# Performance work log

Hardware: AMD Instinct MI355X
Metric: run time of the kernel (lower is better)

The kernel has to match this reference:

```python
import jax, jax.numpy as jnp
import numpy as np

B, S, H, E = 8, 4096, 1024, 8
TEMPERATURE = 1.0


def setup_inputs() -> dict:
    key = jax.random.key(0)
    ks = jax.random.split(key, 7)
    s_h = 1.0 / np.sqrt(H).astype(np.float32)
    s_h2 = 1.0 / np.sqrt(H // 2).astype(np.float32)
    return {
        "hidden_states": jax.random.normal(ks[0], (B, S, H), jnp.float32),
        # routing_network: Linear(H, H//2) -> ReLU -> Linear(H//2, E)
        "W1": jax.random.normal(ks[1], (H, H // 2), jnp.float32) * s_h,
        "b1": jnp.zeros((H // 2,), jnp.float32),
        "W2": jax.random.normal(ks[2], (H // 2, E), jnp.float32) * s_h2,
        "b2": jnp.zeros((E,), jnp.float32),
        # per-expert dense transform (fixed stand-in for torch.randn-per-call)
        "expert_W": jax.random.normal(ks[3], (E, H, H), jnp.float32) * s_h,
        "expert_b": jax.random.normal(ks[4], (E, H), jnp.float32),
    }


def reference(hidden_states, W1, b1, W2, b2, expert_W, expert_b):
    # Routing network -> logits [B, S, E]
    h = jax.nn.relu(jnp.einsum("bsh,hf->bsf", hidden_states, W1) + b1)
    logits = jnp.einsum("bsf,fe->bse", h, W2) + b2
    probs = jax.nn.softmax(logits / TEMPERATURE, axis=-1)
    # top-1 expert per token (scores are NOT applied to output in the original)
    sel = jnp.argmax(probs, axis=-1)  # [B, S] int
    out = jnp.zeros_like(hidden_states)
    for e in range(E):  # small fixed loop over experts
        mask = (sel == e)[..., None].astype(hidden_states.dtype)  # [B, S, 1]
        xe = hidden_states * mask
        ye = jnp.einsum("bsh,hd->bsd", xe, expert_W[e]) + expert_b[e]
        out = out + ye * mask
    return out
```

## Files before the change

kernel.cpp:

```cpp
#include <hip/hip_runtime.h>
#include <hip/hip_bf16.h>
#include <stdint.h>

#define NTOK 32768
#define HD 1024
#define FD 512
#define NEXP 8
#define TAU 0.05f
#define TAU2 4e-4f

typedef __attribute__((ext_vector_type(8))) short short8;
typedef __attribute__((ext_vector_type(4))) float f32x4;

__device__ __forceinline__ short f2bh(float f) {
  uint32_t u = __float_as_uint(f);
  return (short)((u + 0x7fffu + ((u >> 16) & 1u)) >> 16);
}
__device__ __forceinline__ float bh2f(short h) {
  return __uint_as_float(((uint32_t)(uint16_t)h) << 16);
}

__device__ __forceinline__ void gl16(void* lds, const void* g) {
  __builtin_amdgcn_global_load_lds(
      (const __attribute__((address_space(1))) void*)g,
      (__attribute__((address_space(3))) void*)lds, 16, 0, 0);
}

__global__ __launch_bounds__(256) void k_convert(const float* __restrict__ x,
                                                 short* __restrict__ xbf) {
  size_t i = ((size_t)blockIdx.x * 256 + threadIdx.x) * 8;
  f32x4 v0 = *(const f32x4*)(x + i);
  f32x4 v1 = *(const f32x4*)(x + i + 4);
  short8 o;
#pragma unroll
  for (int q = 0; q < 4; ++q) { o[q] = f2bh(v0[q]); o[4 + q] = f2bh(v1[q]); }
  *(short8*)(xbf + i) = o;
}

__global__ __launch_bounds__(256) void k_transpose(
    const float* __restrict__ src, short* __restrict__ dst, int rows, int cols) {
  __shared__ float tile[32][33];
  size_t msz = (size_t)rows * cols;
  src += (size_t)blockIdx.z * msz;
  dst += (size_t)blockIdx.z * msz;
  int c0 = blockIdx.x * 32, r0 = blockIdx.y * 32;
  int tx = threadIdx.x & 31, ty = threadIdx.x >> 5;
#pragma unroll
  for (int i = 0; i < 32; i += 8)
    tile[ty + i][tx] = src[(size_t)(r0 + ty + i) * cols + c0 + tx];
  __syncthreads();
#pragma unroll
  for (int i = 0; i < 32; i += 8)
    dst[(size_t)(c0 + ty + i) * rows + r0 + tx] = f2bh(tile[tx][ty + i]);
}

__global__ __launch_bounds__(256) void k_transpose_split(
    const float* __restrict__ src, short* __restrict__ dstH,
    short* __restrict__ dstL, int rows, int cols) {
  __shared__ float tile[32][33];
  int c0 = blockIdx.x * 32, r0 = blockIdx.y * 32;
  int tx = threadIdx.x & 31, ty = threadIdx.x >> 5;
#pragma unroll
  for (int i = 0; i < 32; i += 8)
    tile[ty + i][tx] = src[(size_t)(r0 + ty + i) * cols + c0 + tx];
  __syncthreads();
#pragma unroll
  for (int i = 0; i < 32; i += 8) {
    float v = tile[tx][ty + i];
    short h = f2bh(v);
    size_t di = (size_t)(c0 + ty + i) * rows + r0 + tx;
    dstH[di] = h;
    dstL[di] = f2bh(v - bh2f(h));
  }
}

template <bool ABF>
__global__ __launch_bounds__(256) void k_gemm1(
    const short* __restrict__ xbf, const float* __restrict__ xf,
    const short* __restrict__ W1T, const float* __restrict__ b1,
    const float* __restrict__ W2, float* __restrict__ part) {
  __shared__ __align__(16) char smem[39168];

  const int tid = threadIdx.x;
  const int lane = tid & 63, wave = tid >> 6;
  const int wr = wave >> 1, wc = wave & 1;
  const int fr = lane & 15, fg = lane >> 4;
  const int bx = ((blockIdx.x & 7) << 5) | (blockIdx.x >> 3);
  const int m0 = bx * 128, n0 = blockIdx.y * 128;
  const int by = blockIdx.y;

  const int off0 = wave * 1024 + lane * 16;
  const int r0 = off0 >> 6, c0 = (off0 & 63) >> 1;
  const int r1 = r0 + 64, c1 = c0;
  const short* b0p = W1T + (size_t)(n0 + r0) * HD + c0;
  const short* b1p = W1T + (size_t)(n0 + r1) * HD + c1;

  const short* a0p = nullptr; const short* a1p = nullptr;
  const float* aF = nullptr;
  int ar = 0, ah = 0;
  if constexpr (ABF) {
    a0p = xbf + (size_t)(m0 + r0) * HD + c0;
    a1p = xbf + (size_t)(m0 + r1) * HD + c1;
  } else {
    ar = tid >> 1; ah = tid & 1;
    aF = xf + (size_t)(m0 + ar) * HD + ah * 16;
  }

  f32x4 acc[4][4];
#pragma unroll
  for (int i = 0; i < 4; ++i)
#pragma unroll
    for (int j = 0; j < 4; ++j) acc[i][j] = (f32x4){0.f, 0.f, 0.f, 0.f};

  auto STAGE = [&](int kt, int b) {
    int k0 = kt * 32;
    gl16(smem + 16384 + b * 8192 + wave * 1024, b0p + k0);
    gl16(smem + 16384 + b * 8192 + 4096 + wave * 1024, b1p + k0);
    if constexpr (ABF) {
      gl16(smem + b * 8192 + wave * 1024, a0p + k0);
      gl16(smem + b * 8192 + 4096 + wave * 1024, a1p + k0);
    } else {
      f32x4 u0 = *(const f32x4*)(aF + k0);
      f32x4 u1 = *(const f32x4*)(aF + k0 + 4);
      f32x4 u2 = *(const f32x4*)(aF + k0 + 8);
      f32x4 u3 = *(const f32x4*)(aF + k0 + 12);
      short8 s0, s1;
#pragma unroll
      for (int q = 0; q < 4; ++q) {
        s0[q] = f2bh(u0[q]); s0[4 + q] = f2bh(u1[q]);
        s1[q] = f2bh(u2[q]); s1[4 + q] = f2bh(u3[q]);
      }
      short* As = (short*)(smem + b * 8192);
      *(short8*)(As + ar * 32 + ah * 16) = s0;
      *(short8*)(As + ar * 32 + ah * 16 + 8) = s1;
    }
  };
  auto COMPUTE = [&](int b) {
    const short* As = (const short*)(smem + b * 8192);
    const short* Bs = (const short*)(smem + 16384 + b * 8192);
    short8 af[4], bf[4];
#pragma unroll
    for (int i = 0; i < 4; ++i) {
      af[i] = *(const short8*)(As + (wr * 64 + i * 16 + fr) * 32 + fg * 8);
      bf[i] = *(const short8*)(Bs + (wc * 64 + i * 16 + fr) * 32 + fg * 8);
    }
#pragma unroll
    for (int i = 0; i < 4; ++i)
#pragma unroll
      for (int j = 0; j < 4; ++j)
        acc[i][j] = __builtin_amdgcn_mfma_f32_16x16x32_bf16(af[i], bf[j], acc[i][j], 0, 0, 0);
  };

  STAGE(0, 0);
  __syncthreads();
#pragma unroll 1
  for (int kt = 0; kt < 32; kt += 2) {
    if (kt + 1 < 32) STAGE(kt + 1, 1);
    COMPUTE(0);
    __syncthreads();
    if (kt + 2 < 32) STAGE(kt + 2, 0);
    COMPUTE(1);
    __syncthreads();
  }

  short* hbf = (short*)smem;
  short* W2b = (short*)(smem + 34816);
  float b1j[4];
#pragma unroll
  for (int j = 0; j < 4; ++j) b1j[j] = b1[n0 + wc * 64 + j * 16 + fr];
  for (int q = tid; q < 2048; q += 256) {
    int col = q >> 7, k = q & 127;
    W2b[col * 136 + k] = (col < 8) ? f2bh(W2[(size_t)(n0 + k) * 8 + col]) : (short)0;
  }
#pragma unroll
  for (int i = 0; i < 4; ++i)
#pragma unroll
    for (int j = 0; j < 4; ++j) {
      int col = wc * 64 + j * 16 + fr;
#pragma unroll
      for (int q = 0; q < 4; ++q)
        hbf[(wr * 64 + i * 16 + fg * 4 + q) * 136 + col] =
            f2bh(fmaxf(acc[i][j][q] + b1j[j], 0.f));
    }
  __syncthreads();
#pragma unroll
  for (int rg = 0; rg < 2; ++rg) {
    int row16 = wave * 32 + rg * 16;
    f32x4 accl = (f32x4){0.f, 0.f, 0.f, 0.f};
#pragma unroll
    for (int kk = 0; kk < 4; ++kk) {
      short8 a = *(const short8*)(hbf + (row16 + fr) * 136 + kk * 32 + fg * 8);
      short8 b = *(const short8*)(W2b + fr * 136 + kk * 32 + fg * 8);
      accl = __builtin_amdgcn_mfma_f32_16x16x32_bf16(a, b, accl, 0, 0, 0);
    }
    if (fr < 8) {
      float* pp = part + (size_t)(m0 + row16 + fg * 4) * 32 + by * 8 + fr;
#pragma unroll
      for (int q = 0; q < 4; ++q) pp[(size_t)q * 32] = accl[q];
    }
  }
}

__global__ __launch_bounds__(256) void k_combine(
    const float* __restrict__ part, const float* __restrict__ b2,
    int* __restrict__ sel, int* __restrict__ flagged, int* __restrict__ nflag) {
  int t = blockIdx.x * 256 + threadIdx.x;
  const float* p = part + (size_t)t * 32;
  float lg[8];
#pragma unroll
  for (int e = 0; e < 8; ++e) lg[e] = p[e] + p[8 + e] + p[16 + e] + p[24 + e] + b2[e];
  int be = 0; float best = lg[0];
#pragma unroll
  for (int e = 1; e < 8; ++e) if (lg[e] > best) { best = lg[e]; be = e; }
  float second = -3.4e38f;
#pragma unroll
  for (int e = 0; e < 8; ++e) if (e != be && lg[e] > second) second = lg[e];
  sel[t] = be;
  if (best - second < TAU) {
    int ix = atomicAdd(nflag, 1);
    if (ix < NTOK) flagged[ix] = t;
  }
}

__global__ __launch_bounds__(256) void k_gemmR(
    const float* __restrict__ x, const short* __restrict__ W1hT,
    const short* __restrict__ W1lT, const float* __restrict__ b1,
    const float* __restrict__ W2, const int* __restrict__ flagged,
    const int* __restrict__ nflag, float* __restrict__ partR) {
  __shared__ __align__(16) char smem[37888];
  __shared__ int toks[128];
  short* Ah = (short*)smem;
  short* Al = (short*)(smem + 8192);

  int nf = *nflag; if (nf > NTOK) nf = NTOK;
  const int m0 = blockIdx.x * 128;
  if (m0 >= nf) return;
  const int tid = threadIdx.x;
  if (tid < 128) {
    int s = m0 + tid;
    toks[tid] = flagged[s < nf ? s : nf - 1];
  }
  __syncthreads();

  const int lane = tid & 63, wave = tid >> 6;
  const int wr = wave >> 1, wc = wave & 1;
  const int fr = lane & 15, fg = lane >> 4;
  const int n0 = blockIdx.y * 128;
  const int by = blockIdx.y;

  const int off0 = wave * 1024 + lane * 16;
  const int off1 = off0 + 4096;
  const int r0 = off0 >> 6, c0 = (off0 & 63) >> 1;
  const int r1 = off1 >> 6, c1 = (off1 & 63) >> 1;
  const short* bh0p = W1hT + (size_t)(n0 + r0) * HD + c0;
  const short* bh1p = W1hT + (size_t)(n0 + r1) * HD + c1;
  const short* bl0p = W1lT + (size_t)(n0 + r0) * HD + c0;
  const short* bl1p = W1lT + (size_t)(n0 + r1) * HD + c1;
  char* ldsBh0 = smem + 16384 + wave * 1024;
  char* ldsBh1 = smem + 16384 + wave * 1024 + 4096;
  char* ldsBl0 = smem + 24576 + wave * 1024;
  char* ldsBl1 = smem + 24576 + wave * 1024 + 4096;
  const int ar = tid >> 1, ah2 = tid & 1;
  const float* aF = x + (size_t)toks[ar] * HD + ah2 * 16;

  f32x4 acc[4][4];
#pragma unroll
  for (int i = 0; i < 4; ++i)
#pragma unroll
    for (int j = 0; j < 4; ++j) acc[i][j] = (f32x4){0.f, 0.f, 0.f, 0.f};

  for (int k0 = 0; k0 < HD; k0 += 32) {
    gl16(ldsBh0, bh0p + k0);
    gl16(ldsBh1, bh1p + k0);
    gl16(ldsBl0, bl0p + k0);
    gl16(ldsBl1, bl1p + k0);
    f32x4 u0 = *(const f32x4*)(aF + k0);
    f32x4 u1 = *(const f32x4*)(aF + k0 + 4);
    f32x4 u2 = *(const f32x4*)(aF + k0 + 8);
    f32x4 u3 = *(const f32x4*)(aF + k0 + 12);
    short8 sh0, sh1, sl0, sl1;
#pragma unroll
    for (int q = 0; q < 4; ++q) {
      { float f = u0[q]; short h = f2bh(f); sh0[q]     = h; sl0[q]     = f2bh(f - bh2f(h)); }
      { float f = u1[q]; short h = f2bh(f); sh0[4 + q] = h; sl0[4 + q] = f2bh(f - bh2f(h)); }
      { float f = u2[q]; short h = f2bh(f); sh1[q]     = h; sl1[q]     = f2bh(f - bh2f(h)); }
      { float f = u3[q]; short h = f2bh(f); sh1[4 + q] = h; sl1[4 + q] = f2bh(f - bh2f(h)); }
    }
    *(short8*)(Ah + ar * 32 + ah2 * 16)     = sh0;
    *(short8*)(Ah + ar * 32 + ah2 * 16 + 8) = sh1;
    *(short8*)(Al + ar * 32 + ah2 * 16)     = sl0;
    *(short8*)(Al + ar * 32 + ah2 * 16 + 8) = sl1;
    __syncthreads();
    short8 af[4], alf[4], bf[4], blf[4];
#pragma unroll
    for (int i = 0; i < 4; ++i) {
      int row = (wr * 64 + i * 16 + fr) * 32 + fg * 8;
      af[i]  = *(const short8*)(Ah + row);
      alf[i] = *(const short8*)(Al + row);
      int rowb = (wc * 64 + i * 16 + fr) * 32 + fg * 8;
      bf[i]  = *(const short8*)((short*)(smem + 16384) + rowb);
      blf[i] = *(const short8*)((short*)(smem + 24576) + rowb);
    }
#pragma unroll
    for (int i = 0; i < 4; ++i)
#pragma unroll
      for (int j = 0; j < 4; ++j) {
        acc[i][j] = __builtin_amdgcn_mfma_f32_16x16x32_bf16(af[i],  bf[j],  acc[i][j], 0, 0, 0);
        acc[i][j] = __builtin_amdgcn_mfma_f32_16x16x32_bf16(af[i],  blf[j], acc[i][j], 0, 0, 0);
        acc[i][j] = __builtin_amdgcn_mfma_f32_16x16x32_bf16(alf[i], bf[j],  acc[i][j], 0, 0, 0);
      }
    __syncthreads();
  }

  float* hl64 = (float*)smem;
  float* W2c  = (float*)(smem + 33024);
  *(f32x4*)(W2c + tid * 4) = *(const f32x4*)(W2 + (size_t)n0 * NEXP + tid * 4);
  float b1j[4];
#pragma unroll
  for (int j = 0; j < 4; ++j) b1j[j] = b1[n0 + wc * 64 + j * 16 + fr];

  for (int p = 0; p < 2; ++p) {
    if (wr == p) {
#pragma unroll
      for (int i = 0; i < 4; ++i)
#pragma unroll
        for (int j = 0; j < 4; ++j) {
          int col = wc * 64 + j * 16 + fr;
#pragma unroll
          for (int q = 0; q < 4; ++q)
            hl64[(i * 16 + fg * 4 + q) * 129 + col] = fmaxf(acc[i][j][q] + b1j[j], 0.f);
        }
    }
    __syncthreads();
    if (tid < 128) {
      int r2 = tid & 63, eh = tid >> 6;
      const float* hrow = hl64 + r2 * 129;
      const float* wcp = W2c + eh * 4;
      float s0 = 0.f, s1 = 0.f, s2 = 0.f, s3 = 0.f;
      for (int f = 0; f < 128; ++f) {
        float hv = hrow[f];
        s0 += hv * wcp[f * 8 + 0];
        s1 += hv * wcp[f * 8 + 1];
        s2 += hv * wcp[f * 8 + 2];
        s3 += hv * wcp[f * 8 + 3];
      }
      float* pp = partR + (size_t)(m0 + p * 64 + r2) * 32 + by * 8 + eh * 4;
      pp[0] = s0; pp[1] = s1; pp[2] = s2; pp[3] = s3;
    }
    __syncthreads();
  }
}

__global__ __launch_bounds__(256) void k_combineR(
    const float* __restrict__ partR, const float* __restrict__ b2,
    const int* __restrict__ flagged, const int* __restrict__ nflag,
    int* __restrict__ sel, int* __restrict__ flagged2, int* __restrict__ nflag2) {
  int nf = *nflag; if (nf > NTOK) nf = NTOK;
  int s = blockIdx.x * 256 + threadIdx.x;
  if (s >= nf) return;
  int t = flagged[s];
  const float* p = partR + (size_t)s * 32;
  float lg[8];
#pragma unroll
  for (int e = 0; e < 8; ++e) lg[e] = p[e] + p[8 + e] + p[16 + e] + p[24 + e] + b2[e];
  int be = 0; float best = lg[0];
#pragma unroll
  for (int e = 1; e < 8; ++e) if (lg[e] > best) { best = lg[e]; be = e; }
  float second = -3.4e38f;
#pragma unroll
  for (int e = 0; e < 8; ++e) if (e != be && lg[e] > second) second = lg[e];
  sel[t] = be;
  if (best - second < TAU2) {
    int ix = atomicAdd(nflag2, 1);
    if (ix < NTOK) flagged2[ix] = t;
  }
}

__global__ __launch_bounds__(256) void k_recomputeB(
    const float* __restrict__ x, const float* __restrict__ W1,
    const float* __restrict__ b1, const float* __restrict__ W2,
    const float* __restrict__ b2, const int* __restrict__ flagged2,
    const int* __restrict__ nflag2, int* __restrict__ sel) {
  __shared__ float xs[1024];
  __shared__ double hs[512];
  __shared__ double red[8][32];
  __shared__ double lgd[8];
  int nf = *nflag2; if (nf > NTOK) nf = NTOK;
  const int tid = threadIdx.x;
  for (int ti = blockIdx.x; ti < nf; ti += gridDim.x) {
    int t = flagged2[ti];
    __syncthreads();
    for (int q = tid; q < 1024; q += 256) xs[q] = x[(size_t)t * HD + q];
    __syncthreads();
    int f0 = tid * 2;
    double a0 = 0.0, a1 = 0.0;
    for (int h = 0; h < 1024; h += 4) {
      float2 w0 = *(const float2*)(W1 + (size_t)(h + 0) * FD + f0);
      float2 w1 = *(const float2*)(W1 + (size_t)(h + 1) * FD + f0);
      float2 w2 = *(const float2*)(W1 + (size_t)(h + 2) * FD + f0);
      float2 w3 = *(const float2*)(W1 + (size_t)(h + 3) * FD + f0);
      double x0 = (double)xs[h], x1 = (double)xs[h + 1];
      double x2 = (double)xs[h + 2], x3 = (double)xs[h + 3];
      a0 += x0 * (double)w0.x; a1 += x0 * (double)w0.y;
      a0 += x1 * (double)w1.x; a1 += x1 * (double)w1.y;
      a0 += x2 * (double)w2.x; a1 += x2 * (double)w2.y;
      a0 += x3 * (double)w3.x; a1 += x3 * (double)w3.y;
    }
    a0 += (double)b1[f0]; a1 += (double)b1[f0 + 1];
    hs[f0]     = a0 > 0.0 ? a0 : 0.0;
    hs[f0 + 1] = a1 > 0.0 ? a1 : 0.0;
    __syncthreads();
    {
      int e = tid >> 5, c = tid & 31;
      int fb = c * 16;
      double s = 0.0;
#pragma unroll
      for (int ff = 0; ff < 16; ++ff)
        s += hs[fb + ff] * (double)W2[(size_t)(fb + ff) * 8 + e];
      red[e][c] = s;
    }
    __syncthreads();
    if (tid < 8) {
      double s = 0.0;
#pragma unroll
      for (int c = 0; c < 32; ++c) s += red[tid][c];
      lgd[tid] = s + (double)b2[tid];
    }
    __syncthreads();
    if (tid == 0) {
      int be = 0; double best = lgd[0];
#pragma unroll
      for (int e = 1; e < 8; ++e) if (lgd[e] > best) { best = lgd[e]; be = e; }
      sel[t] = be;
    }
    __syncthreads();
  }
}

__global__ __launch_bounds__(256) void k_compact(
    const int* __restrict__ sel, int* __restrict__ cnt, int* __restrict__ list) {
  __shared__ int wcnt[4][8];
  __shared__ int woff[4][8];
  __shared__ int bbase[8];
  const int tid = threadIdx.x, lane = tid & 63, wave = tid >> 6;
  const int t = blockIdx.x * 256 + tid;
  const int e = sel[t];
  const unsigned long long ltmask = (1ull << lane) - 1ull;
  int rank = 0;
#pragma unroll
  for (int e2 = 0; e2 < 8; ++e2) {
    unsigned long long m = __ballot(e == e2);
    if (e2 == e) rank = __popcll(m & ltmask);
    if (lane == 0) wcnt[wave][e2] = __popcll(m);
  }
  __syncthreads();
  if (tid < 8) {
    int s0 = wcnt[0][tid], s1 = wcnt[1][tid], s2 = wcnt[2][tid], s3 = wcnt[3][tid];
    woff[0][tid] = 0; woff[1][tid] = s0; woff[2][tid] = s0 + s1; woff[3][tid] = s0 + s1 + s2;
    bbase[tid] = atomicAdd(&cnt[tid], s0 + s1 + s2 + s3);
  }
  __syncthreads();
  list[(size_t)e * NTOK + bbase[e] + woff[wave][e] + rank] = t;
}

__global__ void k_build_desc(const int* __restrict__ cnt, int* __restrict__ desc,
                             int* __restrict__ ntl) {
  if (threadIdx.x == 0 && blockIdx.x == 0) {
    int n = 0;
    for (int e = 0; e < 8; ++e) {
      int m = (cnt[e] + 127) >> 7;
      for (int i = 0; i < m; ++i) desc[n++] = (e << 16) | i;
    }
    *ntl = n;
  }
}

template <bool ABF>
__global__ __launch_bounds__(256) void k_gemm2(
    const short* __restrict__ xbf, const float* __restrict__ xf,
    const short* __restrict__ WexpT, const float* __restrict__ expert_b,
    const int* __restrict__ cnt, const int* __restrict__ list,
    const int* __restrict__ desc, const int* __restrict__ ntl,
    float* __restrict__ out) {
  __shared__ __align__(16) char smem[32768];
  __shared__ int toks[128];
  const int bx = (blockIdx.x % 8) * 33 + blockIdx.x / 8;
  if (bx >= *ntl) return;
  int dsc = desc[bx];
  int e = dsc >> 16, mt = dsc & 0xffff;
  int ce = cnt[e];
  int mb = mt * 128;
  int rows = ce - mb; if (rows > 128) rows = 128;

  const int tid = threadIdx.x;
  if (tid < 128) {
    int idx = mb + tid;
    toks[tid] = list[(size_t)e * NTOK + (idx < ce ? idx : ce - 1)];
  }
  __syncthreads();

  const int lane = tid & 63, wave = tid >> 6;
  const int wr = wave >> 1, wc = wave & 1;
  const int fr = lane & 15, fg = lane >> 4;
  const int n0 = blockIdx.y * 128;

  const int off0 = wave * 1024 + lane * 16;
  const int r0 = off0 >> 6, c0 = (off0 & 63) >> 1;
  const int r1 = r0 + 64, c1 = c0;
  const size_t ebase = (size_t)e << 20;
  const short* b0p = WexpT + ebase + (size_t)(n0 + r0) * HD + c0;
  const short* b1p = WexpT + ebase + (size_t)(n0 + r1) * HD + c1;

  const short* a0p = nullptr; const short* a1p = nullptr;
  const float* aF = nullptr;
  int ar = 0, ah = 0;
  if constexpr (ABF) {
    a0p = xbf + (size_t)toks[r0] * HD + c0;
    a1p = xbf + (size_t)toks[r1] * HD + c1;
  } else {
    ar = tid >> 1; ah = tid & 1;
    aF = xf + (size_t)toks[ar] * HD + ah * 16;
  }

  f32x4 acc[4][4];
#pragma unroll
  for (int i = 0; i < 4; ++i)
#pragma unroll
    for (int j = 0; j < 4; ++j) acc[i][j] = (f32x4){0.f, 0.f, 0.f, 0.f};

  auto STAGE = [&](int kt, int b) {
    int k0 = kt * 32;
    gl16(smem + 16384 + b * 8192 + wave * 1024, b0p + k0);
    gl16(smem + 16384 + b * 8192 + 4096 + wave * 1024, b1p + k0);
    if constexpr (ABF) {
      gl16(smem + b * 8192 + wave * 1024, a0p + k0);
      gl16(smem + b * 8192 + 4096 + wave * 1024, a1p + k0);
    } else {
      f32x4 u0 = *(const f32x4*)(aF + k0);
      f32x4 u1 = *(const f32x4*)(aF + k0 + 4);
      f32x4 u2 = *(const f32x4*)(aF + k0 + 8);
      f32x4 u3 = *(const f32x4*)(aF + k0 + 12);
      short8 s0, s1;
#pragma unroll
      for (int q = 0; q < 4; ++q) {
        s0[q] = f2bh(u0[q]); s0[4 + q] = f2bh(u1[q]);
        s1[q] = f2bh(u2[q]); s1[4 + q] = f2bh(u3[q]);
      }
      short* As = (short*)(smem + b * 8192);
      *(short8*)(As + ar * 32 + ah * 16) = s0;
      *(short8*)(As + ar * 32 + ah * 16 + 8) = s1;
    }
  };
  auto COMPUTE = [&](int b) {
    const short* As = (const short*)(smem + b * 8192);
    const short* Bs = (const short*)(smem + 16384 + b * 8192);
    short8 af[4], bf[4];
#pragma unroll
    for (int i = 0; i < 4; ++i) {
      af[i] = *(const short8*)(As + (wr * 64 + i * 16 + fr) * 32 + fg * 8);
      bf[i] = *(const short8*)(Bs + (wc * 64 + i * 16 + fr) * 32 + fg * 8);
    }
#pragma unroll
    for (int i = 0; i < 4; ++i)
#pragma unroll
      for (int j = 0; j < 4; ++j)
        acc[i][j] = __builtin_amdgcn_mfma_f32_16x16x32_bf16(af[i], bf[j], acc[i][j], 0, 0, 0);
  };

  STAGE(0, 0);
  __syncthreads();
#pragma unroll 1
  for (int kt = 0; kt < 32; kt += 2) {
    if (kt + 1 < 32) STAGE(kt + 1, 1);
    COMPUTE(0);
    __syncthreads();
    if (kt + 2 < 32) STAGE(kt + 2, 0);
    COMPUTE(1);
    __syncthreads();
  }

  float ebv[4];
#pragma unroll
  for (int j = 0; j < 4; ++j) ebv[j] = expert_b[e * HD + n0 + wc * 64 + j * 16 + fr];
#pragma unroll
  for (int i = 0; i < 4; ++i)
#pragma unroll
    for (int j = 0; j < 4; ++j) {
      int col = n0 + wc * 64 + j * 16 + fr;
#pragma unroll
      for (int q = 0; q < 4; ++q) {
        int rr = wr * 64 + i * 16 + fg * 4 + q;
        if (rr < rows) out[(size_t)toks[rr] * HD + col] = acc[i][j][q] + ebv[j];
      }
    }
}

extern "C" void kernel_launch(void* const* d_in, const int* in_sizes, int n_in,
                              void* d_out, int out_size, void* d_ws, size_t ws_size,
                              hipStream_t stream) {
  const float* x  = (const float*)d_in[0];
  const float* W1 = (const float*)d_in[1];
  const float* b1 = (const float*)d_in[2];
  const float* W2 = (const float*)d_in[3];
  const float* b2 = (const float*)d_in[4];
  const float* eW = (const float*)d_in[5];
  const float* eb = (const float*)d_in[6];
  float* out = (float*)d_out;
  char* ws = (char*)d_ws;

  const size_t XBF_BYTES = (size_t)NTOK * HD * 2;
  size_t need_rest = 16777216ull + 1048576 + 4194304 + 131072 * 3 + 1048576 + 4096;
  bool big = ws_size >= XBF_BYTES + need_rest;

  size_t off = 0;
  short* xbf = nullptr;
  if (big) { xbf = (short*)ws; off += XBF_BYTES; }
  short* WexpT  = (short*)(ws + off); off += 16777216;
  short* W1T    = (short*)(ws + off); off += 1048576;
  float* part   = (float*)(ws + off); off += 4194304;
  int* sel      = (int*)(ws + off); off += 131072;
  int* flagged  = (int*)(ws + off); off += 131072;
  int* flagged2 = (int*)(ws + off); off += 131072;
  int* list     = (int*)(ws + off); off += 1048576;
  int* cnt      = (int*)(ws + off); off += 32;
  int* nflag    = (int*)(ws + off); off += 4;
  int* ntl      = (int*)(ws + off); off += 4;
  int* nflag2   = (int*)(ws + off); off += 24;
  int* desc     = (int*)(ws + off); off += 1088;
  if (ws_size < off) return;

  short* W1lT = (short*)list;

  hipMemsetAsync(cnt, 0, 44, stream);

  dim3 b256(256);
  if (big) k_convert<<<dim3(16384), b256, 0, stream>>>(x, xbf);
  k_transpose_split<<<dim3(16, 32), b256, 0, stream>>>(W1, W1T, W1lT, 1024, 512);
  k_transpose<<<dim3(32, 32, 8), b256, 0, stream>>>(eW, WexpT, 1024, 1024);
  if (big)
    k_gemm1<true><<<dim3(256, 4), b256, 0, stream>>>(xbf, nullptr, W1T, b1, W2, part);
  else
    k_gemm1<false><<<dim3(256, 4), b256, 0, stream>>>(nullptr, x, W1T, b1, W2, part);
  k_combine<<<dim3(128), b256, 0, stream>>>(part, b2, sel, flagged, nflag);
  k_gemmR<<<dim3(256, 4), b256, 0, stream>>>(x, W1T, W1lT, b1, W2, flagged, nflag, part);
  k_combineR<<<dim3(128), b256, 0, stream>>>(part, b2, flagged, nflag, sel, flagged2, nflag2);
  k_recomputeB<<<dim3(128), b256, 0, stream>>>(x, W1, b1, W2, b2, flagged2, nflag2, sel);
  k_compact<<<dim3(128), b256, 0, stream>>>(sel, cnt, list);
  k_build_desc<<<dim3(1), dim3(64), 0, stream>>>(cnt, desc, ntl);
  if (big)
    k_gemm2<true><<<dim3(264, 8), b256, 0, stream>>>(xbf, nullptr, WexpT, eb, cnt, list, desc, ntl, out);
  else
    k_gemm2<false><<<dim3(264, 8), b256, 0, stream>>>(nullptr, x, WexpT, eb, cnt, list, desc, ntl, out);
}
```

Baseline: 362.5 us.

## Swizzle LDS tiles and use partial vmcnt waits to overlap loads

Both GEMM kernels now XOR-swizzle the LDS placement of A and B tiles, on the direct-to-LDS load side and on the fragment-read side, to avoid bank conflicts in the MFMA fragment loads. In the bf16 path the barriers become explicit s_waitcnt vmcnt(N) plus s_barrier, so one stage's global-to-LDS loads can stay in flight while the previous stage computes. This adds an extra barrier per half-iteration and relies on exact vmcnt accounting being correct.

```diff
diff --git a/kernel.cpp b/kernel.cpp
--- a/kernel.cpp
+++ b/kernel.cpp
@@ -25,6 +25,19 @@
       (const __attribute__((address_space(1))) void*)g,
       (__attribute__((address_space(3))) void*)lds, 16, 0, 0);
 }
+
+#define WAITBAR(N)                                              \
+  do {                                                          \
+    asm volatile("s_waitcnt vmcnt(" #N ")" ::: "memory");       \
+    __builtin_amdgcn_s_barrier();                               \
+    asm volatile("" ::: "memory");                              \
+  } while (0)
+#define BARO()                                                  \
+  do {                                                          \
+    asm volatile("" ::: "memory");                              \
+    __builtin_amdgcn_s_barrier();                               \
+    asm volatile("" ::: "memory");                              \
+  } while (0)
 
 __global__ __launch_bounds__(256) void k_convert(const float* __restrict__ x,
                                                  short* __restrict__ xbf) {
@@ -89,21 +102,23 @@
   const int m0 = bx * 128, n0 = blockIdx.y * 128;
   const int by = blockIdx.y;
 
-  const int off0 = wave * 1024 + lane * 16;
-  const int r0 = off0 >> 6, c0 = (off0 & 63) >> 1;
-  const int r1 = r0 + 64, c1 = c0;
-  const short* b0p = W1T + (size_t)(n0 + r0) * HD + c0;
-  const short* b1p = W1T + (size_t)(n0 + r1) * HD + c1;
+  const int r0 = wave * 16 + (lane >> 2);
+  const int lsw = (((lane & 3) ^ ((lane >> 3) & 3)) << 3);
+  const short* b0p = W1T + (size_t)(n0 + r0) * HD + lsw;
+  const short* b1p = W1T + (size_t)(n0 + r0 + 64) * HD + lsw;
 
   const short* a0p = nullptr; const short* a1p = nullptr;
   const float* aF = nullptr;
-  int ar = 0, ah = 0;
+  int ar = 0, ah = 0, p0e = 0, p1e = 0;
   if constexpr (ABF) {
-    a0p = xbf + (size_t)(m0 + r0) * HD + c0;
-    a1p = xbf + (size_t)(m0 + r1) * HD + c1;
+    a0p = xbf + (size_t)(m0 + r0) * HD + lsw;
+    a1p = xbf + (size_t)(m0 + r0 + 64) * HD + lsw;
   } else {
     ar = tid >> 1; ah = tid & 1;
     aF = xf + (size_t)(m0 + ar) * HD + ah * 16;
+    int s = (ar >> 1) & 3;
+    p0e = ((2 * ah) ^ s) << 3;
+    p1e = p0e ^ 8;
   }
 
   f32x4 acc[4][4];
@@ -113,7 +128,7 @@
     for (int j = 0; j < 4; ++j) acc[i][j] = (f32x4){0.f, 0.f, 0.f, 0.f};
 
   auto STAGE = [&](int kt, int b) {
-    int k0 = kt * 32;
+    const int k0 = kt * 32;
     gl16(smem + 16384 + b * 8192 + wave * 1024, b0p + k0);
     gl16(smem + 16384 + b * 8192 + 4096 + wave * 1024, b1p + k0);
     if constexpr (ABF) {
@@ -131,36 +146,43 @@
         s1[q] = f2bh(u2[q]); s1[4 + q] = f2bh(u3[q]);
       }
       short* As = (short*)(smem + b * 8192);
-      *(short8*)(As + ar * 32 + ah * 16) = s0;
-      *(short8*)(As + ar * 32 + ah * 16 + 8) = s1;
+      *(short8*)(As + ar * 32 + p0e) = s0;
+      *(short8*)(As + ar * 32 + p1e) = s1;
     }
   };
+  const int csw = (fr >> 1) & 3;
   auto COMPUTE = [&](int b) {
     const short* As = (const short*)(smem + b * 8192);
     const short* Bs = (const short*)(smem + 16384 + b * 8192);
-    short8 af[4], bf[4];
+    short8 af[4], bf4[4];
 #pragma unroll
     for (int i = 0; i < 4; ++i) {
-      af[i] = *(const short8*)(As + (wr * 64 + i * 16 + fr) * 32 + fg * 8);
-      bf[i] = *(const short8*)(Bs + (wc * 64 + i * 16 + fr) * 32 + fg * 8);
+      af[i]  = *(const short8*)(As + (wr * 64 + i * 16 + fr) * 32 + ((fg ^ csw) << 3));
+      bf4[i] = *(const short8*)(Bs + (wc * 64 + i * 16 + fr) * 32 + ((fg ^ csw) << 3));
     }
 #pragma unroll
     for (int i = 0; i < 4; ++i)
 #pragma unroll
       for (int j = 0; j < 4; ++j)
-        acc[i][j] = __builtin_amdgcn_mfma_f32_16x16x32_bf16(af[i], bf[j], acc[i][j], 0, 0, 0);
+        acc[i][j] = __builtin_amdgcn_mfma_f32_16x16x32_bf16(af[i], bf4[j], acc[i][j], 0, 0, 0);
   };
 
   STAGE(0, 0);
-  __syncthreads();
+  if constexpr (ABF) WAITBAR(0); else __syncthreads();
 #pragma unroll 1
   for (int kt = 0; kt < 32; kt += 2) {
-    if (kt + 1 < 32) STAGE(kt + 1, 1);
+    STAGE(kt + 1, 1);
+    if constexpr (ABF) WAITBAR(4); else __syncthreads();
     COMPUTE(0);
-    __syncthreads();
-    if (kt + 2 < 32) STAGE(kt + 2, 0);
+    if constexpr (ABF) BARO(); else __syncthreads();
+    if (kt + 2 < 32) {
+      STAGE(kt + 2, 0);
+      if constexpr (ABF) WAITBAR(4); else __syncthreads();
+    } else {
+      if constexpr (ABF) WAITBAR(0); else __syncthreads();
+    }
     COMPUTE(1);
-    __syncthreads();
+    if constexpr (ABF) BARO(); else __syncthreads();
   }
 
   short* hbf = (short*)smem;
@@ -504,22 +526,24 @@
   const int fr = lane & 15, fg = lane >> 4;
   const int n0 = blockIdx.y * 128;
 
-  const int off0 = wave * 1024 + lane * 16;
-  const int r0 = off0 >> 6, c0 = (off0 & 63) >> 1;
-  const int r1 = r0 + 64, c1 = c0;
+  const int r0 = wave * 16 + (lane >> 2);
+  const int lsw = (((lane & 3) ^ ((lane >> 3) & 3)) << 3);
   const size_t ebase = (size_t)e << 20;
-  const short* b0p = WexpT + ebase + (size_t)(n0 + r0) * HD + c0;
-  const short* b1p = WexpT + ebase + (size_t)(n0 + r1) * HD + c1;
+  const short* b0p = WexpT + ebase + (size_t)(n0 + r0) * HD + lsw;
+  const short* b1p = WexpT + ebase + (size_t)(n0 + r0 + 64) * HD + lsw;
 
   const short* a0p = nullptr; const short* a1p = nullptr;
   const float* aF = nullptr;
-  int ar = 0, ah = 0;
+  int ar = 0, ah = 0, p0e = 0, p1e = 0;
   if constexpr (ABF) {
-    a0p = xbf + (size_t)toks[r0] * HD + c0;
-    a1p = xbf + (size_t)toks[r1] * HD + c1;
+    a0p = xbf + (size_t)toks[r0] * HD + lsw;
+    a1p = xbf + (size_t)toks[r0 + 64] * HD + lsw;
   } else {
     ar = tid >> 1; ah = tid & 1;
     aF = xf + (size_t)toks[ar] * HD + ah * 16;
+    int s = (ar >> 1) & 3;
+    p0e = ((2 * ah) ^ s) << 3;
+    p1e = p0e ^ 8;
   }
 
   f32x4 acc[4][4];
@@ -529,7 +553,7 @@
     for (int j = 0; j < 4; ++j) acc[i][j] = (f32x4){0.f, 0.f, 0.f, 0.f};
 
   auto STAGE = [&](int kt, int b) {
-    int k0 = kt * 32;
+    const int k0 = kt * 32;
     gl16(smem + 16384 + b * 8192 + wave * 1024, b0p + k0);
     gl16(smem + 16384 + b * 8192 + 4096 + wave * 1024, b1p + k0);
     if constexpr (ABF) {
@@ -547,36 +571,43 @@
         s1[q] = f2bh(u2[q]); s1[4 + q] = f2bh(u3[q]);
       }
       short* As = (short*)(smem + b * 8192);
-      *(short8*)(As + ar * 32 + ah * 16) = s0;
-      *(short8*)(As + ar * 32 + ah * 16 + 8) = s1;
+      *(short8*)(As + ar * 32 + p0e) = s0;
+      *(short8*)(As + ar * 32 + p1e) = s1;
     }
   };
+  const int csw = (fr >> 1) & 3;
   auto COMPUTE = [&](int b) {
     const short* As = (const short*)(smem + b * 8192);
     const short* Bs = (const short*)(smem + 16384 + b * 8192);
-    short8 af[4], bf[4];
+    short8 af[4], bf4[4];
 #pragma unroll
     for (int i = 0; i < 4; ++i) {
-      af[i] = *(const short8*)(As + (wr * 64 + i * 16 + fr) * 32 + fg * 8);
-      bf[i] = *(const short8*)(Bs + (wc * 64 + i * 16 + fr) * 32 + fg * 8);
+      af[i]  = *(const short8*)(As + (wr * 64 + i * 16 + fr) * 32 + ((fg ^ csw) << 3));
+      bf4[i] = *(const short8*)(Bs + (wc * 64 + i * 16 + fr) * 32 + ((fg ^ csw) << 3));
     }
 #pragma unroll
     for (int i = 0; i < 4; ++i)
 #pragma unroll
       for (int j = 0; j < 4; ++j)
-        acc[i][j] = __builtin_amdgcn_mfma_f32_16x16x32_bf16(af[i], bf[j], acc[i][j], 0, 0, 0);
+        acc[i][j] = __builtin_amdgcn_mfma_f32_16x16x32_bf16(af[i], bf4[j], acc[i][j], 0, 0, 0);
   };
 
   STAGE(0, 0);
-  __syncthreads();
+  if constexpr (ABF) WAITBAR(0); else __syncthreads();
 #pragma unroll 1
   for (int kt = 0; kt < 32; kt += 2) {
-    if (kt + 1 < 32) STAGE(kt + 1, 1);
+    STAGE(kt + 1, 1);
+    if constexpr (ABF) WAITBAR(4); else __syncthreads();
     COMPUTE(0);
-    __syncthreads();
-    if (kt + 2 < 32) STAGE(kt + 2, 0);
+    if constexpr (ABF) BARO(); else __syncthreads();
+    if (kt + 2 < 32) {
+      STAGE(kt + 2, 0);
+      if constexpr (ABF) WAITBAR(4); else __syncthreads();
+    } else {
+      if constexpr (ABF) WAITBAR(0); else __syncthreads();
+    }
     COMPUTE(1);
-    __syncthreads();
+    if constexpr (ABF) BARO(); else __syncthreads();
   }
 
   float ebv[4];
```

Result: no change. 362.0 us (-0.1%).
